# Kernel optimization log

Hardware: AMD Instinct MI355X
Metric: run time of the kernel (lower is better)

Reference implementation:

```python
import jax, jax.numpy as jnp
import numpy as np

BETA = 0.25  # commitment_beta


def setup_inputs() -> dict:
    key = jax.random.key(0)
    k1, k2 = jax.random.split(key)
    x = jax.random.normal(k1, (16, 256, 32, 32), dtype=jnp.float32)
    # codebook weight: (n_embed + 1, embed_dim); last row is the padding idx (zeros)
    weight = jax.random.normal(k2, (8193, 256), dtype=jnp.float32) * 0.05
    weight = weight.at[-1].set(0.0)
    return {"x": x, "weight": weight}


def reference(x, weight):
    # Eval-mode forward of VectorQuantize2 (accept_image_fmap=True, no EMA update).
    B, C, H, W = x.shape
    xf = jnp.transpose(x, (0, 2, 3, 1)).reshape(B, H * W, C)  # b (h w) c
    emb = weight[:-1]  # [N, C], drop padding row
    # squared euclidean distance; argmin identical to torch.cdist argmin
    d2 = (
        jnp.sum(xf * xf, axis=-1, keepdims=True)
        - 2.0 * jnp.einsum("bnc,kc->bnk", xf, emb)
        + jnp.sum(emb * emb, axis=-1)
    )  # [B, HW, N]
    code = jnp.argmin(d2, axis=-1)  # [B, HW]
    x_q = emb[code]  # [B, HW, C]
    loss = BETA * jnp.mean((jax.lax.stop_gradient(x_q) - xf) ** 2) + jnp.mean(
        (x_q - jax.lax.stop_gradient(xf)) ** 2
    )
    # straight-through estimator
    xq_st = xf + jax.lax.stop_gradient(x_q - xf)
    xq_out = jnp.transpose(xq_st.reshape(B, H, W, C), (0, 3, 1, 2))  # b c h w
    code_out = code.reshape(B, H, W)
    return xq_out, loss, code_out
```

## Files before the change

### kernel.cpp

```cpp
#include <hip/hip_runtime.h>
#include <hip/hip_bf16.h>


#define N_ROWS   16384
#define KCODES   8192
#define DIM      256
#define LOSS_OFF 4194304
#define CODE_OFF 4194305
#define MARGIN_ACC 0.006f

typedef _Float16 half8  __attribute__((ext_vector_type(8)));
typedef _Float16 half4v __attribute__((ext_vector_type(4)));
typedef float    float4v __attribute__((ext_vector_type(4)));
typedef unsigned long long u64;

__device__ __forceinline__ unsigned umax32(unsigned a, unsigned b) { return a > b ? a : b; }
__device__ __forceinline__ unsigned umin32(unsigned a, unsigned b) { return a < b ? a : b; }
__device__ __forceinline__ void gll16(const _Float16* g, _Float16* l) {
  __builtin_amdgcn_global_load_lds((const __attribute__((address_space(1))) void*)g,
                                   (__attribute__((address_space(3))) void*)l, 16, 0, 0);
}


__global__ __launch_bounds__(256) void k_prep(const float* __restrict__ x, _Float16* __restrict__ xh,
                                              const float* __restrict__ wt, _Float16* __restrict__ eh,
                                              float* __restrict__ en2c,
                                              float* __restrict__ lacc, unsigned* __restrict__ cnt) {
  __shared__ __align__(16) _Float16 ls[8192];
  __shared__ float es[32];
  int t = threadIdx.x;
  if (blockIdx.x < 256) {
    if (blockIdx.x == 0 && t == 0) { *lacc = 0.f; *cnt = 0u; }
    int blk  = blockIdx.x;
    int row0 = blk * 64;
    int b    = row0 >> 10;
    int n0   = row0 & 1023;
    const float* xb = x + (size_t)b * 262144 + n0;
    _Float16 (*lsx)[72] = (_Float16(*)[72])ls;
    int c_l = t >> 2;
    int ng0 = t & 3;
    for (int cc = 0; cc < 4; ++cc) {
      if (cc) __syncthreads();
#pragma unroll
      for (int p = 0; p < 4; ++p) {
        int ng = ng0 + 4 * p;
        float4v v = *(const float4v*)&xb[(size_t)(cc * 64 + c_l) * 1024 + ng * 4];
#pragma unroll
        for (int k = 0; k < 4; ++k) lsx[ng * 4 + k][c_l] = (_Float16)v[k];
      }
      __syncthreads();
#pragma unroll
      for (int p2 = 0; p2 < 2; ++p2) {
        int unit = t + 256 * p2;
        int rl64 = unit >> 3, p7 = unit & 7;
        int r = row0 + rl64;
        int kg = p7 ^ (r & 7);
        half8 h = *(const half8*)&lsx[rl64][kg * 8];
        size_t tb = (size_t)(r >> 7) * 32768;
        *(half8*)&xh[tb + (size_t)cc * 8192 + (size_t)(r & 127) * 64 + p7 * 8] = h;
      }
    }
  } else {
    int blk  = blockIdx.x - 256;
    int lane = t & 63, wv = t >> 6;
    int k0 = blk * 32;
    const float* wb = wt + (size_t)k0 * 256;
    for (int i = 0; i < 8; ++i) {
      int lin = i * 1024 + t * 4;
      float4v v = *(const float4v*)&wb[lin];
      half4v h; float ss = 0.f;
#pragma unroll
      for (int j = 0; j < 4; ++j) { h[j] = (_Float16)v[j]; ss = fmaf(v[j], v[j], ss); }
      *(half4v*)&ls[lin] = h;
#pragma unroll
      for (int d = 32; d; d >>= 1) ss += __shfl_xor(ss, d);
      if (lane == 0) es[i * 4 + wv] = ss;
    }
    __syncthreads();
    size_t tb = (size_t)(k0 >> 7) * 32768;
    for (int i = 0; i < 4; ++i) {
      int u = i * 256 + t;
      int code_l = u >> 5;
      int cu = u & 31, chunk = cu >> 3, p = cu & 7;
      int kgl = k0 + code_l;
      int kg = p ^ (kgl & 7);
      half8 h = *(half8*)&ls[code_l * 256 + chunk * 64 + kg * 8];
      *(half8*)&eh[tb + (size_t)chunk * 8192 + (size_t)(kgl & 127) * 64 + p * 8] = h;
    }
    if (t < 32) en2c[k0 + t] = 32.0f - 0.5f * es[t];
  }
}

__global__ __launch_bounds__(256) void k_gemm(const _Float16* __restrict__ xh, const _Float16* __restrict__ eh,
                                              const float* __restrict__ en2c,
                                              u64* __restrict__ top2) {
  __shared__ __align__(16) _Float16 As[8192];
  __shared__ __align__(16) _Float16 Bs[8192];
  int t    = threadIdx.x;
  int bx   = blockIdx.x;
  int by   = blockIdx.y;
  int lane = t & 63, w = t >> 6;
  int wr = w & 1, wc = w >> 1;
  int ln15 = lane & 15, q = lane >> 4;
  int q4 = q * 4;

  const _Float16* Ag = eh + (size_t)bx * 32768;
  const _Float16* Bg = xh + (size_t)by * 32768;

  int kwave = bx * 128 + wr * 64;
  float4v cin[4];
#pragma unroll
  for (int mi = 0; mi < 4; ++mi) cin[mi] = *(const float4v*)&en2c[kwave + mi * 16 + q4];

  float4v acc[4][4];
#pragma unroll
  for (int mi = 0; mi < 4; ++mi)
#pragma unroll
    for (int ni = 0; ni < 4; ++ni) acc[mi][ni] = cin[mi];

  int so = (w * 64 + lane) * 8;
  int lo = w * 512;

  for (int ch = 0; ch < 4; ++ch) {
    if (ch) __syncthreads();
    const _Float16* ac = Ag + ch * 8192;
    const _Float16* bc = Bg + ch * 8192;
#pragma unroll
    for (int i = 0; i < 4; ++i) {
      gll16(ac + i * 2048 + so, As + i * 2048 + lo);
      gll16(bc + i * 2048 + so, Bs + i * 2048 + lo);
    }
    __syncthreads();
#pragma unroll
    for (int ks = 0; ks < 2; ++ks) {
      half8 af[4], bf[4];
#pragma unroll
      for (int mi = 0; mi < 4; ++mi) {
        int row = wr * 64 + mi * 16 + ln15;
        af[mi] = *(const half8*)&As[(row * 8 + ((ks * 4 + q) ^ (row & 7))) * 8];
      }
#pragma unroll
      for (int ni = 0; ni < 4; ++ni) {
        int row = wc * 64 + ni * 16 + ln15;
        bf[ni] = *(const half8*)&Bs[(row * 8 + ((ks * 4 + q) ^ (row & 7))) * 8];
      }
#pragma unroll
      for (int mi = 0; mi < 4; ++mi)
#pragma unroll
        for (int ni = 0; ni < 4; ++ni)
          acc[mi][ni] = __builtin_amdgcn_mfma_f32_16x16x32_f16(af[mi], bf[ni], acc[mi][ni], 0, 0, 0);
    }
  }

  __syncthreads();
  u64* ep = (u64*)(void*)As;
  int ibase = wr * 64 + q4;

#pragma unroll
  for (int ni = 0; ni < 4; ++ni) {
    unsigned hi[8], lo2[8];
#pragma unroll
    for (int j = 0; j < 8; ++j) {
      int mi = j >> 1, rb = (j & 1) * 2;
      unsigned p0 = (__float_as_uint(acc[mi][ni][rb])     & 0xFFFFFF80u) | (unsigned)(ibase + mi * 16 + rb);
      unsigned p1 = (__float_as_uint(acc[mi][ni][rb + 1]) & 0xFFFFFF80u) | (unsigned)(ibase + mi * 16 + rb + 1);
      hi[j] = umax32(p0, p1); lo2[j] = umin32(p0, p1);
    }
#pragma unroll
    for (int st = 4; st; st >>= 1)
#pragma unroll
      for (int j = 0; j < 8; ++j) if (j < st) {
        unsigned nb = umax32(hi[j], hi[j + st]);
        unsigned ns = umax32(umin32(hi[j], hi[j + st]), umax32(lo2[j], lo2[j + st]));
        hi[j] = nb; lo2[j] = ns;
      }
    unsigned b = hi[0], s = lo2[0];
#pragma unroll
    for (int d = 16; d < 64; d <<= 1) {
      unsigned ob = __shfl_xor(b, d);
      unsigned os = __shfl_xor(s, d);
      unsigned ns = umax32(umin32(b, ob), umax32(s, os));
      b = umax32(b, ob); s = ns;
    }
    if (q == 0) {
      int rl = wc * 64 + ni * 16 + ln15;
      ep[rl * 2 + wr] = ((u64)b << 32) | s;
    }
  }
  __syncthreads();
  if (t < 128) {
    u64 A = ep[t * 2 + 0], B = ep[t * 2 + 1];
    unsigned a0 = (unsigned)(A >> 32), a1 = (unsigned)A;
    unsigned b0 = (unsigned)(B >> 32), b1 = (unsigned)B;
    unsigned best = umax32(a0, b0);
    unsigned sec  = umax32(umin32(a0, b0), umax32(a1, b1));
    top2[((size_t)by * 128 + t) * 64 + bx] = ((u64)best << 32) | sec;
  }
}

__global__ __launch_bounds__(256) void k_refine(const u64* __restrict__ top2,
                                                const float* __restrict__ x, const float* __restrict__ w,
                                                int* __restrict__ code, float* __restrict__ out) {
  int t = threadIdx.x, lane = t & 63, wv = t >> 6;
  int row = blockIdx.x * 4 + wv;
  u64 e = top2[(size_t)row * 64 + lane];
  unsigned hi = (unsigned)(e >> 32), lo = (unsigned)e;
  unsigned mx = hi;
#pragma unroll
  for (int d = 1; d < 64; d <<= 1) mx = umax32(mx, __shfl_xor(mx, d));
  float fm = __uint_as_float(mx & 0xFFFFFF80u);
  float th = fm - MARGIN_ACC;
  bool c0 = __uint_as_float(hi & 0xFFFFFF80u) >= th;
  bool c1 = __uint_as_float(lo & 0xFFFFFF80u) >= th;
  u64 bal0 = __ballot(c0), bal1 = __ballot(c1);
  int kbest;
  if (__popcll(bal0) + __popcll(bal1) <= 1) {
    int l0 = __ffsll((unsigned long long)__ballot(hi == mx)) - 1;
    kbest = l0 * 128 + (int)(__shfl(hi, l0) & 127u);
  } else {
    int b = row >> 10, n = row & 1023;
    const float* xr = x + (size_t)b * 262144 + n;
    float4v ex;
#pragma unroll
    for (int i = 0; i < 4; ++i) ex[i] = xr[(size_t)(lane * 4 + i) * 1024];
    double bs = 1e300; int bk = 0x7fffffff;
    for (int pass = 0; pass < 2; ++pass) {
      u64 bal = pass ? bal1 : bal0;
      unsigned src = pass ? lo : hi;
      while (bal) {
        int l = __ffsll((unsigned long long)bal) - 1;
        bal &= bal - 1;
        int kc = l * 128 + (int)(__shfl(src, l) & 127u);
        float4v wv4 = *(const float4v*)&w[(size_t)kc * DIM + lane * 4];
        double s = 0.0;
#pragma unroll
        for (int i = 0; i < 4; ++i) { double ev = (double)wv4[i]; s += ev * (ev - 2.0 * (double)ex[i]); }
#pragma unroll
        for (int d = 1; d < 64; d <<= 1) s += __shfl_xor(s, d);
        if (s < bs || (s == bs && kc < bk)) { bs = s; bk = kc; }
      }
    }
    kbest = bk;
  }
  if (lane == 0) { code[row] = kbest; out[CODE_OFF + row] = (float)kbest; }
}

__global__ __launch_bounds__(256) void k_out(const int* __restrict__ code, const float* __restrict__ w,
                                             const float* __restrict__ x, float* __restrict__ out,
                                             float* __restrict__ lacc, unsigned* __restrict__ cnt) {
  __shared__ float ec[64 * 256];
  int t    = threadIdx.x;
  int lane = t & 63, wv = t >> 6;
  int blk  = blockIdx.x;
  int row0 = blk * 64;
  int b = row0 >> 10, n0 = row0 & 1023;

  int kc = code[row0 + lane];
  const float* wr = w + (size_t)kc * 256;
  int sw = lane & 31;
#pragma unroll 4
  for (int i = 0; i < 16; ++i) {
    int c4 = (wv * 16 + i) * 4;
    float4v v = *(const float4v*)&wr[c4];
#pragma unroll
    for (int k = 0; k < 4; ++k) ec[lane * 256 + ((c4 + k) ^ sw)] = v[k];
  }
  __syncthreads();

  float ls = 0.f;
  const size_t base = (size_t)b * 262144 + n0 + lane;
  for (int j = 0; j < 64; ++j) {
    int c = wv * 64 + j;
    float v = ec[lane * 256 + (c ^ sw)];
    size_t a = base + (size_t)c * 1024;
    float xv = x[a];
    out[a] = v;
    float d = v - xv;
    ls = fmaf(d, d, ls);
  }
#pragma unroll
  for (int d = 32; d; d >>= 1) ls += __shfl_xor(ls, d);
  __syncthreads();
  if (lane == 0) ec[wv] = ls;
  __syncthreads();
  if (t == 0) {
    atomicAdd(lacc, ec[0] + ec[1] + ec[2] + ec[3]);
    __threadfence();
    unsigned old = atomicAdd(cnt, 1u);
    if (old == 255u) {
      __threadfence();
      out[LOSS_OFF] = 1.25f * (*(volatile float*)lacc) / 4194304.0f;
    }
  }
}

extern "C" void kernel_launch(void* const* d_in, const int* in_sizes, int n_in,
                              void* d_out, int out_size, void* d_ws, size_t ws_size,
                              hipStream_t stream) {
  const float* x = (const float*)d_in[0];
  const float* w = (const float*)d_in[1];
  float* out = (float*)d_out;
  char* ws = (char*)d_ws;
  _Float16* xh   = (_Float16*)(ws);
  _Float16* eh   = (_Float16*)(ws + 8388608);
  float*    en2c = (float*)(ws + 12582912);
  u64*      top2 = (u64*)(ws + 12615680);
  int*      codep = (int*)(ws + 21004288);
  float*    lacc = (float*)(ws + 21069824);
  unsigned* cnt  = (unsigned*)(ws + 21069828);

  k_prep<<<512, 256, 0, stream>>>(x, xh, w, eh, en2c, lacc, cnt);
  k_gemm<<<dim3(64, 128), 256, 0, stream>>>(xh, eh, en2c, top2);
  k_refine<<<4096, 256, 0, stream>>>(top2, x, w, codep, out);
  k_out<<<256, 256, 0, stream>>>(codep, w, x, out, lacc, cnt);
}
```

Measured before the change: 180.3 us.

## Fuse top-2 refine into output kernel and transpose top2 layout

Result: no change. 178.1 us (-1.2%).

```diff
diff --git a/kernel.cpp b/kernel.cpp
--- a/kernel.cpp
+++ b/kernel.cpp
@@ -194,84 +194,75 @@
     unsigned b0 = (unsigned)(B >> 32), b1 = (unsigned)B;
     unsigned best = umax32(a0, b0);
     unsigned sec  = umax32(umin32(a0, b0), umax32(a1, b1));
-    top2[((size_t)by * 128 + t) * 64 + bx] = ((u64)best << 32) | sec;
-  }
-}
-
-__global__ __launch_bounds__(256) void k_refine(const u64* __restrict__ top2,
-                                                const float* __restrict__ x, const float* __restrict__ w,
-                                                int* __restrict__ code, float* __restrict__ out) {
-  int t = threadIdx.x, lane = t & 63, wv = t >> 6;
-  int row = blockIdx.x * 4 + wv;
-  u64 e = top2[(size_t)row * 64 + lane];
-  unsigned hi = (unsigned)(e >> 32), lo = (unsigned)e;
-  unsigned mx = hi;
-#pragma unroll
-  for (int d = 1; d < 64; d <<= 1) mx = umax32(mx, __shfl_xor(mx, d));
-  float fm = __uint_as_float(mx & 0xFFFFFF80u);
-  float th = fm - MARGIN_ACC;
-  bool c0 = __uint_as_float(hi & 0xFFFFFF80u) >= th;
-  bool c1 = __uint_as_float(lo & 0xFFFFFF80u) >= th;
-  u64 bal0 = __ballot(c0), bal1 = __ballot(c1);
-  int kbest;
-  if (__popcll(bal0) + __popcll(bal1) <= 1) {
-    int l0 = __ffsll((unsigned long long)__ballot(hi == mx)) - 1;
-    kbest = l0 * 128 + (int)(__shfl(hi, l0) & 127u);
-  } else {
-    int b = row >> 10, n = row & 1023;
-    const float* xr = x + (size_t)b * 262144 + n;
-    float4v ex;
-#pragma unroll
-    for (int i = 0; i < 4; ++i) ex[i] = xr[(size_t)(lane * 4 + i) * 1024];
-    double bs = 1e300; int bk = 0x7fffffff;
-    for (int pass = 0; pass < 2; ++pass) {
-      u64 bal = pass ? bal1 : bal0;
-      unsigned src = pass ? lo : hi;
-      while (bal) {
-        int l = __ffsll((unsigned long long)bal) - 1;
-        bal &= bal - 1;
-        int kc = l * 128 + (int)(__shfl(src, l) & 127u);
-        float4v wv4 = *(const float4v*)&w[(size_t)kc * DIM + lane * 4];
-        double s = 0.0;
-#pragma unroll
-        for (int i = 0; i < 4; ++i) { double ev = (double)wv4[i]; s += ev * (ev - 2.0 * (double)ex[i]); }
-#pragma unroll
-        for (int d = 1; d < 64; d <<= 1) s += __shfl_xor(s, d);
-        if (s < bs || (s == bs && kc < bk)) { bs = s; bk = kc; }
-      }
-    }
-    kbest = bk;
-  }
-  if (lane == 0) { code[row] = kbest; out[CODE_OFF + row] = (float)kbest; }
-}
-
-__global__ __launch_bounds__(256) void k_out(const int* __restrict__ code, const float* __restrict__ w,
-                                             const float* __restrict__ x, float* __restrict__ out,
+    top2[(size_t)bx * 16384 + (size_t)by * 128 + t] = ((u64)best << 32) | sec;
+  }
+}
+
+__global__ __launch_bounds__(512) void k_out(const u64* __restrict__ top2,
+                                             const float* __restrict__ x, const float* __restrict__ w,
+                                             float* __restrict__ out,
                                              float* __restrict__ lacc, unsigned* __restrict__ cnt) {
-  __shared__ float ec[64 * 256];
+  __shared__ float ect[256 * 65];
+  __shared__ float part[8];
   int t    = threadIdx.x;
   int lane = t & 63, wv = t >> 6;
   int blk  = blockIdx.x;
   int row0 = blk * 64;
   int b = row0 >> 10, n0 = row0 & 1023;
 
-  int kc = code[row0 + lane];
-  const float* wr = w + (size_t)kc * 256;
-  int sw = lane & 31;
-#pragma unroll 4
-  for (int i = 0; i < 16; ++i) {
-    int c4 = (wv * 16 + i) * 4;
-    float4v v = *(const float4v*)&wr[c4];
-#pragma unroll
-    for (int k = 0; k < 4; ++k) ec[lane * 256 + ((c4 + k) ^ sw)] = v[k];
+  for (int j = 0; j < 8; ++j) {
+    int rl  = wv * 8 + j;
+    int row = row0 + rl;
+    u64 e = top2[(size_t)lane * 16384 + row];
+    unsigned hi = (unsigned)(e >> 32), lo = (unsigned)e;
+    unsigned mx = hi;
+#pragma unroll
+    for (int d = 1; d < 64; d <<= 1) mx = umax32(mx, __shfl_xor(mx, d));
+    float fm = __uint_as_float(mx & 0xFFFFFF80u);
+    float th = fm - MARGIN_ACC;
+    bool c0 = __uint_as_float(hi & 0xFFFFFF80u) >= th;
+    bool c1 = __uint_as_float(lo & 0xFFFFFF80u) >= th;
+    u64 bal0 = __ballot(c0), bal1 = __ballot(c1);
+    int kbest;
+    if (__popcll(bal0) + __popcll(bal1) <= 1) {
+      int l0 = __ffsll((unsigned long long)__ballot(hi == mx)) - 1;
+      kbest = l0 * 128 + (int)(__shfl(hi, l0) & 127u);
+    } else {
+      const float* xr = x + (size_t)b * 262144 + (row & 1023);
+      float4v ex;
+#pragma unroll
+      for (int i = 0; i < 4; ++i) ex[i] = xr[(size_t)(lane * 4 + i) * 1024];
+      double bs = 1e300; int bk = 0x7fffffff;
+      for (int pass = 0; pass < 2; ++pass) {
+        u64 bal = pass ? bal1 : bal0;
+        unsigned src = pass ? lo : hi;
+        while (bal) {
+          int l = __ffsll((unsigned long long)bal) - 1;
+          bal &= bal - 1;
+          int kc = l * 128 + (int)(__shfl(src, l) & 127u);
+          float4v wv4 = *(const float4v*)&w[(size_t)kc * DIM + lane * 4];
+          double s = 0.0;
+#pragma unroll
+          for (int i = 0; i < 4; ++i) { double ev = (double)wv4[i]; s += ev * (ev - 2.0 * (double)ex[i]); }
+#pragma unroll
+          for (int d = 1; d < 64; d <<= 1) s += __shfl_xor(s, d);
+          if (s < bs || (s == bs && kc < bk)) { bs = s; bk = kc; }
+        }
+      }
+      kbest = bk;
+    }
+    if (lane == 0) out[CODE_OFF + row] = (float)kbest;
+    const float* wrow = w + (size_t)kbest * 256;
+#pragma unroll
+    for (int i = 0; i < 4; ++i) ect[(i * 64 + lane) * 65 + rl] = wrow[i * 64 + lane];
   }
   __syncthreads();
 
   float ls = 0.f;
   const size_t base = (size_t)b * 262144 + n0 + lane;
-  for (int j = 0; j < 64; ++j) {
-    int c = wv * 64 + j;
-    float v = ec[lane * 256 + (c ^ sw)];
+  for (int j = 0; j < 32; ++j) {
+    int c = wv * 32 + j;
+    float v = ect[c * 65 + lane];
     size_t a = base + (size_t)c * 1024;
     float xv = x[a];
     out[a] = v;
@@ -280,11 +271,11 @@
   }
 #pragma unroll
   for (int d = 32; d; d >>= 1) ls += __shfl_xor(ls, d);
-  __syncthreads();
-  if (lane == 0) ec[wv] = ls;
+  if (lane == 0) part[wv] = ls;
   __syncthreads();
   if (t == 0) {
-    atomicAdd(lacc, ec[0] + ec[1] + ec[2] + ec[3]);
+    float s = part[0] + part[1] + part[2] + part[3] + part[4] + part[5] + part[6] + part[7];
+    atomicAdd(lacc, s);
     __threadfence();
     unsigned old = atomicAdd(cnt, 1u);
     if (old == 255u) {
@@ -305,12 +296,10 @@
   _Float16* eh   = (_Float16*)(ws + 8388608);
   float*    en2c = (float*)(ws + 12582912);
   u64*      top2 = (u64*)(ws + 12615680);
-  int*      codep = (int*)(ws + 21004288);
-  float*    lacc = (float*)(ws + 21069824);
-  unsigned* cnt  = (unsigned*)(ws + 21069828);
+  float*    lacc = (float*)(ws + 21004288);
+  unsigned* cnt  = (unsigned*)(ws + 21004292);
 
   k_prep<<<512, 256, 0, stream>>>(x, xh, w, eh, en2c, lacc, cnt);
   k_gemm<<<dim3(64, 128), 256, 0, stream>>>(xh, eh, en2c, top2);
-  k_refine<<<4096, 256, 0, stream>>>(top2, x, w, codep, out);
-  k_out<<<256, 256, 0, stream>>>(codep, w, x, out, lacc, cnt);
-}
+  k_out<<<256, 512, 0, stream>>>(top2, x, w, out, lacc, cnt);
+}
```
